# Optimization experiments

Measured on AMD Instinct MI355X. Metric: run time of the kernel, lower is better.

The kernel has to match this reference:

```python
import jax, jax.numpy as jnp
import numpy as np

B, T, C = 2, 2048, 2048
N_HEAD, N_KV_HEAD = 16, 4
HEAD_DIM = C // N_HEAD  # 128
EPS = 1e-6


def rms_norm(x):
    # no learned scale, normalize over head_dim (last axis)
    return x * jax.lax.rsqrt(jnp.mean(jnp.square(x), axis=-1, keepdims=True) + EPS)


def apply_rotary_emb(x, cos, sin):
    # x: [B, T, H, D]; cos/sin: [T, D/2]  (rotate-half RoPE)
    x1, x2 = jnp.split(x, 2, axis=-1)
    c = cos[None, :, None, :]
    s = sin[None, :, None, :]
    return jnp.concatenate([x1 * c - x2 * s, x1 * s + x2 * c], axis=-1)


def setup_inputs() -> dict:
    key = jax.random.key(0)
    ks = jax.random.split(key, 6)
    x = jax.random.normal(ks[0], (B, T, C), dtype=jnp.float32)
    # real rotary tables: theta = 10000^{-2i/D}
    inv_freq = 1.0 / (10000.0 ** (jnp.arange(0, HEAD_DIM, 2, dtype=jnp.float32) / HEAD_DIM))
    angles = jnp.arange(T, dtype=jnp.float32)[:, None] * inv_freq[None, :]  # [T, D/2]
    cos, sin = jnp.cos(angles), jnp.sin(angles)
    std = 0.02
    Wq = jax.random.normal(ks[1], (C, N_HEAD * HEAD_DIM), dtype=jnp.float32) * std
    Wk = jax.random.normal(ks[2], (C, N_KV_HEAD * HEAD_DIM), dtype=jnp.float32) * std
    Wv = jax.random.normal(ks[3], (C, N_KV_HEAD * HEAD_DIM), dtype=jnp.float32) * std
    Wp = jax.random.normal(ks[4], (C, C), dtype=jnp.float32) * std
    return {"x": x, "cos": cos, "sin": sin, "Wq": Wq, "Wk": Wk, "Wv": Wv, "Wp": Wp}


def reference(x, cos, sin, Wq, Wk, Wv, Wp):
    Bx, Tx, Cx = x.shape
    q = (x @ Wq).reshape(Bx, Tx, N_HEAD, HEAD_DIM)
    k = (x @ Wk).reshape(Bx, Tx, N_KV_HEAD, HEAD_DIM)
    v = (x @ Wv).reshape(Bx, Tx, N_KV_HEAD, HEAD_DIM)
    q = rms_norm(apply_rotary_emb(q, cos, sin))
    k = rms_norm(apply_rotary_emb(k, cos, sin))
    # module scales q by 1/sqrt(D) AND nn.dot_product_attention scales again
    q = q * (1.0 / jnp.sqrt(HEAD_DIM))
    # GQA head repeat
    n_rep = N_HEAD // N_KV_HEAD
    k = jnp.repeat(k, n_rep, axis=2)  # [B, T, H, D]
    v = jnp.repeat(v, n_rep, axis=2)
    scores = jnp.einsum("bthd,bshd->bhts", q, k) / jnp.sqrt(jnp.asarray(HEAD_DIM, x.dtype))
    causal = jnp.tril(jnp.ones((Tx, Tx), dtype=bool))  # key <= query
    scores = jnp.where(causal[None, None, :, :], scores, jnp.finfo(scores.dtype).min)
    probs = jax.nn.softmax(scores, axis=-1)
    y = jnp.einsum("bhts,bshd->bthd", probs, v).reshape(Bx, Tx, Cx)
    return y @ Wp
```

## Files before the change

kernel.cpp:

```cpp
#include <hip/hip_runtime.h>
#include <hip/hip_bf16.h>
#include <math.h>

#define B_  2
#define T_  2048
#define C_  2048
#define NH_ 16
#define NKV_ 4
#define HD_ 128
#define NREP_ (NH_/NKV_)

#define QKVLD 3072
#define KOFF  2048
#define VOFF  2560

#define QSCALE 0.01127105500694502f

typedef __bf16 bf16x8 __attribute__((ext_vector_type(8)));
typedef float  f32x4  __attribute__((ext_vector_type(4)));
typedef float  f32x16 __attribute__((ext_vector_type(16)));

__device__ inline void gload_lds16(const void* g, void* l) {
    __builtin_amdgcn_global_load_lds((const __attribute__((address_space(1))) void*)g,
                                     (__attribute__((address_space(3))) void*)l, 16, 0, 0);
}

__global__ __launch_bounds__(256) void cast_bf16(const float* __restrict__ src,
                                                 __bf16* __restrict__ dst)
{
    size_t i = ((size_t)blockIdx.x * 256 + threadIdx.x) * 8;
    float4 a = *(const float4*)&src[i];
    float4 b = *(const float4*)&src[i + 4];
    union { __bf16 h[8]; uint4 u; } pk;
    pk.h[0] = (__bf16)a.x; pk.h[1] = (__bf16)a.y; pk.h[2] = (__bf16)a.z; pk.h[3] = (__bf16)a.w;
    pk.h[4] = (__bf16)b.x; pk.h[5] = (__bf16)b.y; pk.h[6] = (__bf16)b.z; pk.h[7] = (__bf16)b.w;
    *(uint4*)&dst[i] = pk.u;
}

__global__ __launch_bounds__(256) void wtrans_qkv(const float* __restrict__ Wq,
                                                  const float* __restrict__ Wk,
                                                  const float* __restrict__ Wv,
                                                  __bf16* __restrict__ dst)
{
    __shared__ float tl[32][33];
    int ct = blockIdx.x;
    int k0 = blockIdx.y * 32;
    const float* src;
    int ncols, c0, dr0;
    if (ct < 64)      { src = Wq; ncols = 2048; c0 = ct * 32;        dr0 = ct * 32; }
    else if (ct < 80) { src = Wk; ncols = 512;  c0 = (ct - 64) * 32; dr0 = KOFF + (ct - 64) * 32; }
    else              { src = Wv; ncols = 512;  c0 = (ct - 80) * 32; dr0 = VOFF + (ct - 80) * 32; }

    int tid = threadIdx.x;
    int r  = tid >> 3;
    int c4 = (tid & 7) * 4;
    float4 v = *(const float4*)&src[(size_t)(k0 + r) * ncols + c0 + c4];
    tl[r][c4] = v.x; tl[r][c4 + 1] = v.y; tl[r][c4 + 2] = v.z; tl[r][c4 + 3] = v.w;
    __syncthreads();
    union { __bf16 h[4]; uint2 u; } pk;
#pragma unroll
    for (int j = 0; j < 4; ++j) pk.h[j] = (__bf16)tl[c4 + j][r];
    *(uint2*)&dst[(size_t)(dr0 + r) * 2048 + k0 + c4] = pk.u;
}

__global__ __launch_bounds__(256) void wtrans(const float* __restrict__ src,
                                              __bf16* __restrict__ dst, int ncols)
{
    __shared__ float tl[32][33];
    int n0 = blockIdx.x * 32;
    int k0 = blockIdx.y * 32;
    int tid = threadIdx.x;
    int r  = tid >> 3;
    int c4 = (tid & 7) * 4;
    float4 v = *(const float4*)&src[(size_t)(k0 + r) * ncols + n0 + c4];
    tl[r][c4] = v.x; tl[r][c4 + 1] = v.y; tl[r][c4 + 2] = v.z; tl[r][c4 + 3] = v.w;
    __syncthreads();
    union { __bf16 h[4]; uint2 u; } pk;
#pragma unroll
    for (int j = 0; j < 4; ++j) pk.h[j] = (__bf16)tl[c4 + j][r];
    *(uint2*)&dst[(size_t)(n0 + r) * 2048 + k0 + c4] = pk.u;
}

template<typename TOUT>
__global__ __launch_bounds__(256) void gemm_bt(const __bf16* __restrict__ A,
                                               const __bf16* __restrict__ Bt,
                                               TOUT* __restrict__ C,
                                               int M, int N, int K, int ldc)
{
    __shared__ __bf16 As[2][128 * 32];
    __shared__ __bf16 Bs[2][128 * 32];

    const int tid  = threadIdx.x;
    const int wv   = tid >> 6;
    const int lane = tid & 63;
    const int grp  = lane >> 4;
    const int id16 = lane & 15;
    const int wr   = wv >> 1;
    const int wc   = wv & 1;

    const int row0 = blockIdx.y * 128;
    const int col0 = blockIdx.x * 128;

    const int sm = tid >> 2;
    const int sk = (tid & 3) << 3;

    const __bf16* ga0 = A  + (size_t)(row0 + sm) * K + sk;
    const __bf16* ga1 = A  + (size_t)(row0 + 64 + sm) * K + sk;
    const __bf16* gb0 = Bt + (size_t)(col0 + sm) * K + sk;
    const __bf16* gb1 = Bt + (size_t)(col0 + 64 + sm) * K + sk;

    f32x4 acc[4][4];
    const f32x4 fz = {0.f, 0.f, 0.f, 0.f};
#pragma unroll
    for (int i = 0; i < 4; ++i)
#pragma unroll
        for (int j = 0; j < 4; ++j) acc[i][j] = fz;

    const int nk = K >> 5;

    {
        __bf16* a0 = &As[0][wv << 9];
        __bf16* b0 = &Bs[0][wv << 9];
        gload_lds16(ga0, a0);
        gload_lds16(ga1, a0 + 2048);
        gload_lds16(gb0, b0);
        gload_lds16(gb1, b0 + 2048);
    }

    for (int kt = 0; kt < nk; ++kt) {
        const int bufc = kt & 1;
        asm volatile("s_waitcnt vmcnt(0)" ::: "memory");
        __syncthreads();

        if (kt + 1 < nk) {
            const int kb = (kt + 1) << 5;
            __bf16* a0 = &As[1 - bufc][wv << 9];
            __bf16* b0 = &Bs[1 - bufc][wv << 9];
            gload_lds16(ga0 + kb, a0);
            gload_lds16(ga1 + kb, a0 + 2048);
            gload_lds16(gb0 + kb, b0);
            gload_lds16(gb1 + kb, b0 + 2048);
        }

        bf16x8 af[4], bfr[4];
#pragma unroll
        for (int i = 0; i < 4; ++i)
            af[i] = *(const bf16x8*)&As[bufc][((wr << 6) + (i << 4) + id16) * 32 + (grp << 3)];
#pragma unroll
        for (int j = 0; j < 4; ++j)
            bfr[j] = *(const bf16x8*)&Bs[bufc][((wc << 6) + (j << 4) + id16) * 32 + (grp << 3)];
#pragma unroll
        for (int i = 0; i < 4; ++i)
#pragma unroll
            for (int j = 0; j < 4; ++j)
                acc[i][j] = __builtin_amdgcn_mfma_f32_16x16x32_bf16(af[i], bfr[j], acc[i][j], 0, 0, 0);
    }

#pragma unroll
    for (int i = 0; i < 4; ++i) {
        int gr = row0 + (wr << 6) + (i << 4) + (grp << 2);
#pragma unroll
        for (int j = 0; j < 4; ++j) {
            int gc = col0 + (wc << 6) + (j << 4) + id16;
#pragma unroll
            for (int r = 0; r < 4; ++r) {
                if constexpr (sizeof(TOUT) == 4)
                    C[(size_t)(gr + r) * ldc + gc] = acc[i][j][r];
                else
                    C[(size_t)(gr + r) * ldc + gc] = (TOUT)acc[i][j][r];
            }
        }
    }
}

__global__ __launch_bounds__(256) void rope_rms_b(__bf16* __restrict__ base,
                                                  const float* __restrict__ cosb,
                                                  const float* __restrict__ sinb,
                                                  int nheads, float scale)
{
    int wid  = blockIdx.x * 4 + (threadIdx.x >> 6);
    int lane = threadIdx.x & 63;
    int bt = wid / nheads;
    int hd = wid % nheads;
    int t  = bt % T_;

    __bf16* p = base + (size_t)bt * QKVLD + hd * HD_;
    float c = cosb[t * 64 + lane];
    float s = sinb[t * 64 + lane];
    float x1 = (float)p[lane];
    float x2 = (float)p[lane + 64];
    float r1 = x1 * c - x2 * s;
    float r2 = x1 * s + x2 * c;
    float ss = r1 * r1 + r2 * r2;
#pragma unroll
    for (int off = 32; off; off >>= 1) ss += __shfl_xor(ss, off, 64);
    float inv = rsqrtf(ss * (1.f / 128.f) + 1e-6f) * scale;
    p[lane]      = (__bf16)(r1 * inv);
    p[lane + 64] = (__bf16)(r2 * inv);
}

__global__ __launch_bounds__(256) void vtrans(const __bf16* __restrict__ qkv,
                                              __bf16* __restrict__ vt)
{
    __shared__ __bf16 tl[32][HD_ + 8];
    int bx  = blockIdx.x;
    int st  = bx & 63;
    int bkv = bx >> 6;
    int b = bkv >> 2, kv = bkv & 3;
    int s0 = st << 5;
    int tid = threadIdx.x;
    {
        int s = tid >> 3;
        int d = (tid & 7) << 4;
        const __bf16* src = qkv + (size_t)(b * T_ + s0 + s) * QKVLD + VOFF + kv * HD_ + d;
        *(bf16x8*)&tl[s][d]     = *(const bf16x8*)src;
        *(bf16x8*)&tl[s][d + 8] = *(const bf16x8*)(src + 8);
    }
    __syncthreads();
    {
        int d  = tid >> 1;
        int sh = (tid & 1) << 4;
        __bf16 tmp[16];
#pragma unroll
        for (int j = 0; j < 16; ++j) tmp[j] = tl[sh + j][d];
        __bf16* dst = vt + ((size_t)(b * NKV_ + kv) * HD_ + d) * T_ + s0 + sh;
        *(bf16x8*)dst       = *(bf16x8*)&tmp[0];
        *(bf16x8*)(dst + 8) = *(bf16x8*)&tmp[8];
    }
}

__global__ __launch_bounds__(256, 2) void attn32(const __bf16* __restrict__ qkv,
                                                 const __bf16* __restrict__ vbT,
                                                 __bf16* __restrict__ y)
{
    __shared__ __bf16 Ks[2][64 * 128];
    __shared__ __bf16 Vs[2][64 * 128];

    const int tid  = threadIdx.x;
    const int wv   = tid >> 6;
    const int lane = tid & 63;
    const int l31  = lane & 31;
    const int h32  = lane >> 5;

    const int bx    = blockIdx.x;
    const int jslot = bx >> 5;
    const int bh    = bx & 31;
    const int b     = bh >> 4;
    const int h     = bh & 15;
    const int kv    = h >> 2;
    const int jj    = (jslot < 8) ? (15 - jslot) : (jslot - 8);

    const int NT  = 2 * jj + 2;
    const int qw0 = jj * 128 + wv * 32;
    const int qme = qw0 + l31;

    size_t koff[4], voff[4];
#pragma unroll
    for (int i = 0; i < 4; ++i) {
        int r  = (wv * 4 + i) * 4 + (lane >> 4);
        int c  = lane & 15;
        int cs = c ^ (r & 15);
        koff[i] = (size_t)r * (QKVLD * 2) + (size_t)cs * 16;
        int d   = r + ((cs >> 3) << 6);
        voff[i] = (size_t)d * (T_ * 2) + (size_t)(cs & 7) * 16;
    }
    const char* kg = (const char*)(qkv + (size_t)b * T_ * QKVLD + KOFF + kv * HD_);
    const char* vg = (const char*)(vbT + ((size_t)(b * NKV_ + kv) * HD_) * T_);

    bf16x8 qf[8];
    {
        const __bf16* qp = qkv + (size_t)(b * T_ + qw0 + l31) * QKVLD + h * HD_ + h32 * 8;
#pragma unroll
        for (int s = 0; s < 8; ++s) qf[s] = *(const bf16x8*)(qp + s * 16);
    }

    f32x16 o[4];
#pragma unroll
    for (int dt = 0; dt < 4; ++dt)
#pragma unroll
        for (int r = 0; r < 16; ++r) o[dt][r] = 0.f;
    float l_p = 0.f;

    {
        __bf16* kl = &Ks[0][(wv * 4) * 512];
        __bf16* vl = &Vs[0][(wv * 4) * 512];
#pragma unroll
        for (int i = 0; i < 4; ++i) gload_lds16(kg + koff[i], kl + i * 512);
#pragma unroll
        for (int i = 0; i < 4; ++i) gload_lds16(vg + voff[i], vl + i * 512);
    }

    for (int tt = 0; tt < NT; ++tt) {
        const int bufc = tt & 1;
        asm volatile("s_waitcnt vmcnt(0)" ::: "memory");
        __syncthreads();

        if (tt + 1 < NT) {
            const char* kp = kg + (size_t)(tt + 1) * (64 * QKVLD * 2);
            const char* vp = vg + (size_t)(tt + 1) * (64 * 2);
            __bf16* kl = &Ks[1 - bufc][(wv * 4) * 512];
            __bf16* vl = &Vs[1 - bufc][(wv * 4) * 512];
#pragma unroll
            for (int i = 0; i < 4; ++i) gload_lds16(kp + koff[i], kl + i * 512);
#pragma unroll
            for (int i = 0; i < 4; ++i) gload_lds16(vp + voff[i], vl + i * 512);
        }

        const int s0 = tt << 6;
        if (s0 > qw0 + 31) continue;

        f32x16 S0, S1;
#pragma unroll
        for (int r = 0; r < 16; ++r) { S0[r] = 0.f; S1[r] = 0.f; }
        const __bf16* Kb = Ks[bufc];
        __builtin_amdgcn_s_setprio(1);
#pragma unroll
        for (int s = 0; s < 8; ++s) {
            int ch = s * 2 + h32;
            bf16x8 kf0 = *(const bf16x8*)&Kb[l31 * 128 + ((ch ^ (l31 & 15)) << 3)];
            bf16x8 kf1 = *(const bf16x8*)&Kb[(32 + l31) * 128 + ((ch ^ (l31 & 15)) << 3)];
            S0 = __builtin_amdgcn_mfma_f32_32x32x16_bf16(kf0, qf[s], S0, 0, 0, 0);
            S1 = __builtin_amdgcn_mfma_f32_32x32x16_bf16(kf1, qf[s], S1, 0, 0, 0);
        }
        __builtin_amdgcn_s_setprio(0);

        const bool domask = (s0 + 63 > qw0);
        uint w[16];
#pragma unroll
        for (int i = 0; i < 8; ++i) {
            const int r0 = 2 * i;
            float e0 = exp2f(S0[r0]);
            float e1 = exp2f(S0[r0 + 1]);
            if (domask) {
                int k0 = s0 + (r0 & 3) + 8 * (r0 >> 2) + 4 * h32;
                if (k0     > qme) e0 = 0.f;
                if (k0 + 1 > qme) e1 = 0.f;
            }
            l_p += e0 + e1;
            union { __bf16 h2[2]; uint u; } pk;
            pk.h2[0] = (__bf16)e0; pk.h2[1] = (__bf16)e1;
            w[i] = pk.u;
        }
#pragma unroll
        for (int i = 0; i < 8; ++i) {
            const int r0 = 2 * i;
            float e0 = exp2f(S1[r0]);
            float e1 = exp2f(S1[r0 + 1]);
            if (domask) {
                int k0 = s0 + 32 + (r0 & 3) + 8 * (r0 >> 2) + 4 * h32;
                if (k0     > qme) e0 = 0.f;
                if (k0 + 1 > qme) e1 = 0.f;
            }
            l_p += e0 + e1;
            union { __bf16 h2[2]; uint u; } pk;
            pk.h2[0] = (__bf16)e0; pk.h2[1] = (__bf16)e1;
            w[8 + i] = pk.u;
        }

        uint sw[16];
#pragma unroll
        for (int i = 0; i < 16; ++i) sw[i] = (uint)__shfl_xor((int)w[i], 32, 64);

        union U8 { uint u[4]; bf16x8 v; };
        bf16x8 pf[4];
#pragma unroll
        for (int ks = 0; ks < 4; ++ks) {
            const int bsel = ((ks >> 1) << 3) + ((ks & 1) << 2);
            U8 t;
            if (h32 == 0) {
                t.u[0] = w[bsel];      t.u[1] = w[bsel + 1];
                t.u[2] = sw[bsel];     t.u[3] = sw[bsel + 1];
            } else {
                t.u[0] = sw[bsel + 2]; t.u[1] = sw[bsel + 3];
                t.u[2] = w[bsel + 2];  t.u[3] = w[bsel + 3];
            }
            pf[ks] = t.v;
        }

        const __bf16* Vb = Vs[bufc];
        __builtin_amdgcn_s_setprio(1);
#pragma unroll
        for (int dt = 0; dt < 4; ++dt) {
            const int vrow = ((dt & 1) << 5) + l31;
            const int cb   = (dt >> 1) << 3;
#pragma unroll
            for (int ks = 0; ks < 4; ++ks) {
                int ch = cb + ks * 2 + h32;
                bf16x8 vf = *(const bf16x8*)&Vb[vrow * 128 + ((ch ^ (vrow & 15)) << 3)];
                o[dt] = __builtin_amdgcn_mfma_f32_32x32x16_bf16(vf, pf[ks], o[dt], 0, 0, 0);
            }
        }
        __builtin_amdgcn_s_setprio(0);
    }

    float l  = l_p + __shfl_xor(l_p, 32, 64);
    float inv = 1.f / l;
    __bf16* yp = y + (size_t)(b * T_ + qw0 + l31) * C_ + h * HD_;
#pragma unroll
    for (int dt = 0; dt < 4; ++dt)
#pragma unroll
        for (int g = 0; g < 4; ++g) {
            union { __bf16 h4[4]; uint2 u; } pk;
#pragma unroll
            for (int e = 0; e < 4; ++e) pk.h4[e] = (__bf16)(o[dt][4 * g + e] * inv);
            *(uint2*)&yp[dt * 32 + 8 * g + 4 * h32] = pk.u;
        }
}

extern "C" void kernel_launch(void* const* d_in, const int* in_sizes, int n_in,
                              void* d_out, int out_size, void* d_ws, size_t ws_size,
                              hipStream_t stream)
{
    const float* x    = (const float*)d_in[0];
    const float* cosb = (const float*)d_in[1];
    const float* sinb = (const float*)d_in[2];
    const float* Wq   = (const float*)d_in[3];
    const float* Wk   = (const float*)d_in[4];
    const float* Wv   = (const float*)d_in[5];
    const float* Wp   = (const float*)d_in[6];
    float* out = (float*)d_out;

    const int M = B_ * T_;

    char* w = (char*)d_ws;
    __bf16* xb    = (__bf16*)w;  w += (size_t)M * C_ * 2;
    __bf16* qkv   = (__bf16*)w;  w += (size_t)M * QKVLD * 2;
    __bf16* wqkvT = (__bf16*)w;  w += (size_t)QKVLD * C_ * 2;
    __bf16* wpT   = (__bf16*)w;  w += (size_t)C_ * C_ * 2;
    __bf16* vt    = (__bf16*)w;  w += (size_t)M * NKV_ * HD_ * 2;
    __bf16* y     = (__bf16*)w;

    cast_bf16<<<(M * C_) / 2048, 256, 0, stream>>>(x, xb);
    wtrans_qkv<<<dim3(96, C_ / 32), 256, 0, stream>>>(Wq, Wk, Wv, wqkvT);
    wtrans<<<dim3(C_ / 32, C_ / 32), 256, 0, stream>>>(Wp, wpT, C_);

    gemm_bt<__bf16><<<dim3(QKVLD / 128, M / 128), 256, 0, stream>>>(xb, wqkvT, qkv, M, QKVLD, C_, QKVLD);

    rope_rms_b<<<(M * NH_) / 4, 256, 0, stream>>>(qkv, cosb, sinb, NH_, QSCALE);
    rope_rms_b<<<(M * NKV_) / 4, 256, 0, stream>>>(qkv + KOFF, cosb, sinb, NKV_, 1.0f);

    vtrans<<<B_ * NKV_ * (T_ / 32), 256, 0, stream>>>(qkv, vt);

    attn32<<<512, 256, 0, stream>>>(qkv, vt, y);

    gemm_bt<float><<<dim3(C_ / 128, M / 128), 256, 0, stream>>>(y, wpT, out, M, C_, C_, C_);
}
```

Measured before the change: 332.7 us.

## Split causal attention work evenly across blocks with partial outputs and combine kernel

Each block now runs exactly 17 key tiles. Role-0 blocks handle the first part of a high query tile. Role-1 blocks finish that high tile, store its partial output, then process a low query tile. Partial unnormalized outputs and row sums are written to fp32 scratch (reusing xb and wqkvT regions), and a new combine kernel sums them and normalizes into y. This is meant to remove tail imbalance from uneven causal work per block, at the cost of extra fp32 partial traffic, doubled Q register usage and an extra kernel launch.

```diff
diff --git a/kernel.cpp b/kernel.cpp
--- a/kernel.cpp
+++ b/kernel.cpp
@@ -231,7 +231,11 @@
 
 __global__ __launch_bounds__(256, 2) void attn32(const __bf16* __restrict__ qkv,
                                                  const __bf16* __restrict__ vbT,
-                                                 __bf16* __restrict__ y)
+                                                 __bf16* __restrict__ y,
+                                                 float* __restrict__ pOA,
+                                                 float* __restrict__ pOB,
+                                                 float* __restrict__ pLA,
+                                                 float* __restrict__ pLB)
 {
     __shared__ __bf16 Ks[2][64 * 128];
     __shared__ __bf16 Vs[2][64 * 128];
@@ -242,17 +246,23 @@
     const int l31  = lane & 31;
     const int h32  = lane >> 5;
 
-    const int bx    = blockIdx.x;
-    const int jslot = bx >> 5;
-    const int bh    = bx & 31;
-    const int b     = bh >> 4;
-    const int h     = bh & 15;
-    const int kv    = h >> 2;
-    const int jj    = (jslot < 8) ? (15 - jslot) : (jslot - 8);
-
-    const int NT  = 2 * jj + 2;
-    const int qw0 = jj * 128 + wv * 32;
-    const int qme = qw0 + l31;
+    const int bx   = blockIdx.x;
+    const int bh   = bx & 31;
+    const int role = (bx >> 5) & 1;
+    const int p    = bx >> 6;
+    const int b    = bh >> 4;
+    const int h    = bh & 15;
+    const int kv   = h >> 2;
+    const int slot = p * 32 + bh;
+
+    const int hi  = 15 - p;
+    const int lo  = p;
+    const int tts = role ? (15 - 2 * p) : 99;
+
+    auto KT = [&](int t) { return role ? (t < tts ? 17 + t : t - tts) : t; };
+
+    int qw0 = hi * 128 + wv * 32;
+    int qme = qw0 + l31;
 
     size_t koff[4], voff[4];
 #pragma unroll
@@ -267,11 +277,14 @@
     const char* kg = (const char*)(qkv + (size_t)b * T_ * QKVLD + KOFF + kv * HD_);
     const char* vg = (const char*)(vbT + ((size_t)(b * NKV_ + kv) * HD_) * T_);
 
-    bf16x8 qf[8];
+    bf16x8 qf[8], qf2[8];
     {
-        const __bf16* qp = qkv + (size_t)(b * T_ + qw0 + l31) * QKVLD + h * HD_ + h32 * 8;
+        const __bf16* qp = qkv + (size_t)(b * T_ + hi * 128 + wv * 32 + l31) * QKVLD + h * HD_ + h32 * 8;
 #pragma unroll
         for (int s = 0; s < 8; ++s) qf[s] = *(const bf16x8*)(qp + s * 16);
+        const __bf16* qp2 = qkv + (size_t)(b * T_ + lo * 128 + wv * 32 + l31) * QKVLD + h * HD_ + h32 * 8;
+#pragma unroll
+        for (int s = 0; s < 8; ++s) qf2[s] = *(const bf16x8*)(qp2 + s * 16);
     }
 
     f32x16 o[4];
@@ -281,23 +294,43 @@
         for (int r = 0; r < 16; ++r) o[dt][r] = 0.f;
     float l_p = 0.f;
 
+#define STORE_PARTIAL(PO, PL)                                                   \
+    {                                                                           \
+        float lsum = l_p + __shfl_xor(l_p, 32, 64);                             \
+        int qloc = wv * 32 + l31;                                               \
+        float* po = (PO) + ((size_t)slot * 128 + qloc) * 128;                   \
+        _Pragma("unroll")                                                       \
+        for (int dt = 0; dt < 4; ++dt)                                          \
+            _Pragma("unroll")                                                   \
+            for (int g = 0; g < 4; ++g) {                                       \
+                float4 f = {o[dt][4 * g + 0], o[dt][4 * g + 1],                 \
+                            o[dt][4 * g + 2], o[dt][4 * g + 3]};                \
+                *(float4*)&po[dt * 32 + 8 * g + 4 * h32] = f;                   \
+            }                                                                   \
+        if (h32 == 0) (PL)[slot * 128 + qloc] = lsum;                           \
+    }
+
     {
+        int kt0 = KT(0);
+        const char* kp = kg + (size_t)kt0 * (64 * QKVLD * 2);
+        const char* vp = vg + (size_t)kt0 * (64 * 2);
         __bf16* kl = &Ks[0][(wv * 4) * 512];
         __bf16* vl = &Vs[0][(wv * 4) * 512];
 #pragma unroll
-        for (int i = 0; i < 4; ++i) gload_lds16(kg + koff[i], kl + i * 512);
-#pragma unroll
-        for (int i = 0; i < 4; ++i) gload_lds16(vg + voff[i], vl + i * 512);
-    }
-
-    for (int tt = 0; tt < NT; ++tt) {
+        for (int i = 0; i < 4; ++i) gload_lds16(kp + koff[i], kl + i * 512);
+#pragma unroll
+        for (int i = 0; i < 4; ++i) gload_lds16(vp + voff[i], vl + i * 512);
+    }
+
+    for (int tt = 0; tt < 17; ++tt) {
         const int bufc = tt & 1;
         asm volatile("s_waitcnt vmcnt(0)" ::: "memory");
         __syncthreads();
 
-        if (tt + 1 < NT) {
-            const char* kp = kg + (size_t)(tt + 1) * (64 * QKVLD * 2);
-            const char* vp = vg + (size_t)(tt + 1) * (64 * 2);
+        if (tt + 1 < 17) {
+            int kn = KT(tt + 1);
+            const char* kp = kg + (size_t)kn * (64 * QKVLD * 2);
+            const char* vp = vg + (size_t)kn * (64 * 2);
             __bf16* kl = &Ks[1 - bufc][(wv * 4) * 512];
             __bf16* vl = &Vs[1 - bufc][(wv * 4) * 512];
 #pragma unroll
@@ -306,7 +339,20 @@
             for (int i = 0; i < 4; ++i) gload_lds16(vp + voff[i], vl + i * 512);
         }
 
-        const int s0 = tt << 6;
+        if (role && tt == tts) {
+            STORE_PARTIAL(pOB, pLB);
+#pragma unroll
+            for (int dt = 0; dt < 4; ++dt)
+#pragma unroll
+                for (int r = 0; r < 16; ++r) o[dt][r] = 0.f;
+            l_p = 0.f;
+#pragma unroll
+            for (int s = 0; s < 8; ++s) qf[s] = qf2[s];
+            qw0 = lo * 128 + wv * 32;
+            qme = qw0 + l31;
+        }
+
+        const int s0 = KT(tt) << 6;
         if (s0 > qw0 + 31) continue;
 
         f32x16 S0, S1;
@@ -393,18 +439,59 @@
         __builtin_amdgcn_s_setprio(0);
     }
 
-    float l  = l_p + __shfl_xor(l_p, 32, 64);
-    float inv = 1.f / l;
-    __bf16* yp = y + (size_t)(b * T_ + qw0 + l31) * C_ + h * HD_;
-#pragma unroll
-    for (int dt = 0; dt < 4; ++dt)
-#pragma unroll
-        for (int g = 0; g < 4; ++g) {
-            union { __bf16 h4[4]; uint2 u; } pk;
-#pragma unroll
-            for (int e = 0; e < 4; ++e) pk.h4[e] = (__bf16)(o[dt][4 * g + e] * inv);
-            *(uint2*)&yp[dt * 32 + 8 * g + 4 * h32] = pk.u;
-        }
+    if (role == 0) {
+        STORE_PARTIAL(pOA, pLA);
+    } else {
+        float l  = l_p + __shfl_xor(l_p, 32, 64);
+        float inv = 1.f / l;
+        __bf16* yp = y + (size_t)(b * T_ + qw0 + l31) * C_ + h * HD_;
+#pragma unroll
+        for (int dt = 0; dt < 4; ++dt)
+#pragma unroll
+            for (int g = 0; g < 4; ++g) {
+                union { __bf16 h4[4]; uint2 u; } pk;
+#pragma unroll
+                for (int e = 0; e < 4; ++e) pk.h4[e] = (__bf16)(o[dt][4 * g + e] * inv);
+                *(uint2*)&yp[dt * 32 + 8 * g + 4 * h32] = pk.u;
+            }
+    }
+#undef STORE_PARTIAL
+}
+
+__global__ __launch_bounds__(256) void attn_combine(const float* __restrict__ pOA,
+                                                    const float* __restrict__ pOB,
+                                                    const float* __restrict__ pLA,
+                                                    const float* __restrict__ pLB,
+                                                    __bf16* __restrict__ y)
+{
+    int slot = blockIdx.x;
+    int p  = slot >> 5, bh = slot & 31;
+    int b  = bh >> 4,   h  = bh & 15;
+    int hi = 15 - p;
+    int t  = threadIdx.x;
+    int q  = t >> 1;
+    int dh = (t & 1) << 6;
+
+    float inv = 1.f / (pLA[slot * 128 + q] + pLB[slot * 128 + q]);
+    size_t base = ((size_t)slot * 128 + q) * 128 + dh;
+    __bf16* yp = y + (size_t)(b * T_ + hi * 128 + q) * C_ + h * HD_ + dh;
+#pragma unroll
+    for (int d0 = 0; d0 < 64; d0 += 8) {
+        float4 a0 = *(const float4*)&pOA[base + d0];
+        float4 a1 = *(const float4*)&pOA[base + d0 + 4];
+        float4 b0 = *(const float4*)&pOB[base + d0];
+        float4 b1 = *(const float4*)&pOB[base + d0 + 4];
+        union { __bf16 h8[8]; uint4 u; } pk;
+        pk.h8[0] = (__bf16)((a0.x + b0.x) * inv);
+        pk.h8[1] = (__bf16)((a0.y + b0.y) * inv);
+        pk.h8[2] = (__bf16)((a0.z + b0.z) * inv);
+        pk.h8[3] = (__bf16)((a0.w + b0.w) * inv);
+        pk.h8[4] = (__bf16)((a1.x + b1.x) * inv);
+        pk.h8[5] = (__bf16)((a1.y + b1.y) * inv);
+        pk.h8[6] = (__bf16)((a1.z + b1.z) * inv);
+        pk.h8[7] = (__bf16)((a1.w + b1.w) * inv);
+        *(uint4*)&yp[d0] = pk.u;
+    }
 }
 
 extern "C" void kernel_launch(void* const* d_in, const int* in_sizes, int n_in,
@@ -428,7 +515,11 @@
     __bf16* wqkvT = (__bf16*)w;  w += (size_t)QKVLD * C_ * 2;
     __bf16* wpT   = (__bf16*)w;  w += (size_t)C_ * C_ * 2;
     __bf16* vt    = (__bf16*)w;  w += (size_t)M * NKV_ * HD_ * 2;
-    __bf16* y     = (__bf16*)w;
+    __bf16* y     = (__bf16*)w;  w += (size_t)M * C_ * 2;
+    float*  pOB   = (float*)w;
+    float*  pOA   = (float*)xb;
+    float*  pLA   = (float*)wqkvT;
+    float*  pLB   = pLA + 8 * 32 * 128;
 
     cast_bf16<<<(M * C_) / 2048, 256, 0, stream>>>(x, xb);
     wtrans_qkv<<<dim3(96, C_ / 32), 256, 0, stream>>>(Wq, Wk, Wv, wqkvT);
@@ -441,7 +532,8 @@
 
     vtrans<<<B_ * NKV_ * (T_ / 32), 256, 0, stream>>>(qkv, vt);
 
-    attn32<<<512, 256, 0, stream>>>(qkv, vt, y);
+    attn32<<<512, 256, 0, stream>>>(qkv, vt, y, pOA, pOB, pLA, pLB);
+    attn_combine<<<256, 256, 0, stream>>>(pOA, pOB, pLA, pLB, y);
 
     gemm_bt<float><<<dim3(C_ / 128, M / 128), 256, 0, stream>>>(y, wpT, out, M, C_, C_, C_);
 }
```

New measurement: 327.1 us. Within noise of the previous version (-1.7%).
